# Kernel optimization log

Hardware: AMD Instinct MI355X
Metric: run time of the kernel (lower is better)

## Reference

```python
import jax, jax.numpy as jnp
import numpy as np

HEADS, DIM_HEAD = 4, 32
EAF_LAMBDA, EAF_ZMAX = 1.0, 4.0
MIN_SIGMA, MAX_SIGMA = 1.0, 8.0

def _gen_grid(h, w):
    xs = np.linspace(0.0, 1.0, w, dtype=np.float32)
    ys = np.linspace(0.0, 1.0, h, dtype=np.float32)
    gy, gx = np.meshgrid(ys, xs, indexing='ij')
    return np.stack([gx, gy, np.ones_like(gx)], 0)  # [3,h,w]

def setup_inputs():
    key = jax.random.key(0)
    ks = jax.random.split(key, 12)
    B, N, C, D = 4, 6, 128, 128
    Hb, Wb, fh, fw = 25, 25, 24, 48
    inner = HEADS * DIM_HEAD
    # BEV ego-plane grid (same math as BEVEmbedding with bev 200x200, 100m, 3 decoder blocks)
    g = _gen_grid(Hb, Wb)
    g[0] *= 200.0
    g[1] *= 200.0
    V = np.array([[0., -2., 100.], [-2., 0., 100.], [0., 0., 1.]], dtype=np.float32)
    bev_grid = (np.linalg.inv(V) @ g.reshape(3, -1)).reshape(3, Hb, Wb)
    # image plane pixel grid (buffer), scaled to 480x224 image
    ip = _gen_grid(fh, fw)[None]
    ip[:, 0] *= 480.0
    ip[:, 1] *= 224.0
    # cam->world extrinsics: 6 surround cameras on a ring
    E_inv = np.zeros((B, N, 4, 4), dtype=np.float32)
    for n in range(N):
        yaw = 2.0 * np.pi * n / N
        c, s = np.cos(yaw), np.sin(yaw)
        E_inv[:, n, :3, :3] = np.array([[c, -s, 0.], [s, c, 0.], [0., 0., 1.]], dtype=np.float32)
        E_inv[:, n, :3, 3] = np.array([2. * c, 2. * s, 1.6], dtype=np.float32)
        E_inv[:, n, 3, 3] = 1.0
    Kmat = np.array([[260., 0., 240.], [0., 260., 112.], [0., 0., 1.]], dtype=np.float32)
    I_inv = np.broadcast_to(np.linalg.inv(Kmat), (B, N, 3, 3)).astype(np.float32).copy()
    w = lambda k, shape: 0.02 * jax.random.normal(k, shape, dtype=jnp.float32)
    return dict(
        x=jax.random.normal(ks[0], (B, D, Hb, Wb), dtype=jnp.float32),
        feature=jax.random.normal(ks[1], (B, N, C, fh, fw), dtype=jnp.float32),
        I_inv=jnp.asarray(I_inv), E_inv=jnp.asarray(E_inv),
        bev_grid=jnp.asarray(bev_grid), image_plane=jnp.asarray(ip),
        bn_v_g=jnp.ones(C), bn_v_b=jnp.zeros(C), bn_v_m=jnp.zeros(C), bn_v_var=jnp.ones(C),
        conv_v_w=w(ks[2], (D, C)),
        bn_k_g=jnp.ones(C), bn_k_b=jnp.zeros(C), bn_k_m=jnp.zeros(C), bn_k_var=jnp.ones(C),
        conv_k_w=w(ks[3], (D, C)),
        ln_q_g=jnp.ones(D), ln_q_b=jnp.zeros(D),
        ln_k_g=jnp.ones(D), ln_k_b=jnp.zeros(D),
        ln_v_g=jnp.ones(D), ln_v_b=jnp.zeros(D),
        Wq=w(ks[4], (inner, D)), bq=jnp.zeros(inner),
        Wk=w(ks[5], (inner, D)), bk=jnp.zeros(inner),
        Wv=w(ks[6], (inner, D)), bv=jnp.zeros(inner),
        Wo=w(ks[7], (D, inner)), bo=jnp.zeros(D),
        ln_pre_g=jnp.ones(D), ln_pre_b=jnp.zeros(D),
        W1=w(ks[8], (2 * D, D)), b1=jnp.zeros(2 * D),
        W2=w(ks[9], (D, 2 * D)), b2=jnp.zeros(D),
        ln_post_g=jnp.ones(D), ln_post_b=jnp.zeros(D),
    )

def _ln(x, g, b):
    m = x.mean(-1, keepdims=True)
    v = ((x - m) ** 2).mean(-1, keepdims=True)
    return (x - m) * jax.lax.rsqrt(v + 1e-5) * g + b

def _bn_relu_conv(f, g, b, mu, var, Wc):
    # inference BatchNorm2d -> ReLU -> 1x1 Conv (no bias)
    f = (f - mu[None, :, None, None]) * (jax.lax.rsqrt(var + 1e-5) * g)[None, :, None, None] + b[None, :, None, None]
    f = jax.nn.relu(f)
    return jnp.einsum('bchw,dc->bdhw', f, Wc)

def reference(x, feature, I_inv, E_inv, bev_grid, image_plane,
              bn_v_g, bn_v_b, bn_v_m, bn_v_var, conv_v_w,
              bn_k_g, bn_k_b, bn_k_m, bn_k_var, conv_k_w,
              ln_q_g, ln_q_b, ln_k_g, ln_k_b, ln_v_g, ln_v_b,
              Wq, bq, Wk, bk, Wv, bv, Wo, bo,
              ln_pre_g, ln_pre_b, W1, b1, W2, b2, ln_post_g, ln_post_b):
    B, N, C, fh, fw = feature.shape
    _, D, Hb, Wb = x.shape
    Q = Hb * Wb
    Kp = fh * fw
    feat = feature.reshape(B * N, C, fh, fw)
    val = _bn_relu_conv(feat, bn_v_g, bn_v_b, bn_v_m, bn_v_var, conv_v_w)
    keyf = _bn_relu_conv(feat, bn_k_g, bn_k_b, bn_k_m, bn_k_var, conv_k_w)
    v = val.reshape(B, N, D, fh, fw)
    k = keyf.reshape(B, N, D, fh, fw)
    # ---- EAF weights ----
    xy = bev_grid[:2].reshape(2, Q).T                      # [Q,2]
    ones = jnp.ones((Q, 1), dtype=bev_grid.dtype)
    P0 = jnp.concatenate([xy, 0.0 * ones, ones], -1)       # [Q,4] z=0
    P1 = jnp.concatenate([xy, EAF_ZMAX * ones, ones], -1)  # [Q,4] z=zmax
    E = jnp.linalg.inv(E_inv)                              # world->cam
    P0c = jnp.einsum('bnij,qj->bnqi', E, P0)
    P1c = jnp.einsum('bnij,qj->bnqi', E, P1)
    Icam = jnp.linalg.inv(I_inv)
    p0 = jnp.einsum('bnij,bnqj->bnqi', Icam, P0c[..., :3])
    p1 = jnp.einsum('bnij,bnqj->bnqi', Icam, P1c[..., :3])
    p0 = p0 / (p0[..., 2:3] + 1e-8)
    p1 = p1 / (p1[..., 2:3] + 1e-8)
    l = jnp.cross(p0, p1)                                  # epipolar line [B,N,Q,3]
    denom = jnp.maximum(jnp.sqrt(l[..., 0] ** 2 + l[..., 1] ** 2), 1e-8)
    l_hat = l / denom[..., None]
    x_img = image_plane[0].reshape(3, Kp).T                # [K,3]
    d = jnp.abs(jnp.einsum('bnqj,kj->bnqk', l_hat, x_img))
    # adaptive lambda_{q,i}
    cam_xy = E_inv[..., :2, 3]                             # [B,N,2]
    vec = xy[None, None] - cam_xy[:, :, None]              # [B,N,Q,2]
    dist = jnp.linalg.norm(vec, axis=-1) + 1e-6
    dist_max = dist.max(axis=(1, 2), keepdims=True) + 1e-6
    dist_norm = jnp.clip(dist / dist_max, 0.0, 1.0)
    sigma = MAX_SIGMA - dist_norm * (MAX_SIGMA - MIN_SIGMA)
    lambda_qi = 1.0 / (sigma + 1e-6)
    scale_w = (EAF_LAMBDA * lambda_qi) ** 2                # [B,N,Q]
    Wmask = jnp.exp(-scale_w[..., None] * d ** 2)          # [B,N,Q,K]
    W_logits = Wmask.transpose(0, 2, 1, 3).reshape(B, Q, N * Kp)
    # ---- cross attention (EAF weight multiplied into logits pre-softmax) ----
    qt = x.reshape(B, D, Q).transpose(0, 2, 1)             # [B,Q,D]
    kt = k.transpose(0, 1, 3, 4, 2).reshape(B, N * Kp, D)
    vt = v.transpose(0, 1, 3, 4, 2).reshape(B, N * Kp, D)
    qp = _ln(qt, ln_q_g, ln_q_b) @ Wq.T + bq
    kp = _ln(kt, ln_k_g, ln_k_b) @ Wk.T + bk
    vp = _ln(vt, ln_v_g, ln_v_b) @ Wv.T + bv
    qh = qp.reshape(B, Q, HEADS, DIM_HEAD).transpose(0, 2, 1, 3)
    kh = kp.reshape(B, N * Kp, HEADS, DIM_HEAD).transpose(0, 2, 1, 3)
    vh = vp.reshape(B, N * Kp, HEADS, DIM_HEAD).transpose(0, 2, 1, 3)
    logits = jnp.einsum('bhqd,bhkd->bhqk', qh, kh) * (DIM_HEAD ** -0.5)
    logits = logits * W_logits[:, None]                    # broadcast over heads
    attn = jax.nn.softmax(logits, axis=-1)
    out = jnp.einsum('bhqk,bhkd->bhqd', attn, vh)
    out = out.transpose(0, 2, 1, 3).reshape(B, Q, HEADS * DIM_HEAD)
    out = out @ Wo.T + bo                                  # [B,Q,D]
    z = out + qt                                           # skip = x
    z = _ln(z, ln_pre_g, ln_pre_b)
    z = z + (jax.nn.gelu(z @ W1.T + b1, approximate=False) @ W2.T + b2)
    z = _ln(z, ln_post_g, ln_post_b)
    return z.transpose(0, 2, 1).reshape(B, D, Hb, Wb)
```

## Files before the change

kernel.cpp:

```cpp
#include <hip/hip_runtime.h>
#include <hip/hip_bf16.h>

typedef unsigned short u16;
typedef __attribute__((ext_vector_type(8))) short short8v;
typedef __attribute__((ext_vector_type(4))) float f32x4;
typedef __attribute__((ext_vector_type(2))) __fp16 fp16x2;

#define B_   4
#define N_   6
#define Q_   625
#define QPAD 640
#define KP_  1152
#define NK_  6912
#define NKB  216
#define NSPLIT 24
#define KSEG (NK_/NSPLIT)
#define FHW  1152
#define LOG2E 1.4426950408889634f
#define LOG2_LOG2E 0.5287663729448977f

__device__ __forceinline__ float bfu(unsigned int u16v){ return __uint_as_float(u16v << 16); }
__device__ __forceinline__ unsigned int f2bfu(float f){
  unsigned int u = __float_as_uint(f);
  return (u + 0x7fffu + ((u>>16)&1u)) >> 16;
}
__device__ __forceinline__ float exp2a(float x){
  float r; asm("v_exp_f32 %0, %1" : "=v"(r) : "v"(x)); return r;
}
__device__ __forceinline__ unsigned cvtpk_bf16(float lo, float hi){
  unsigned r; asm("v_cvt_pk_bf16_f32 %0, %1, %2" : "=v"(r) : "v"(lo), "v"(hi)); return r;
}
__device__ __forceinline__ unsigned cvtpk_f16(float lo, float hi){
  union { fp16x2 h; unsigned u; } c;
  c.h = __builtin_amdgcn_cvt_pkrtz(lo, hi);
  return c.u;
}
__device__ __forceinline__ float ldfeat(const void* p, size_t i, bool isbf){
  return isbf ? bfu((unsigned)reinterpret_cast<const u16*>(p)[i])
              : reinterpret_cast<const float*>(p)[i];
}
union U4S8 { uint4 u; short8v s; };
union H2U { unsigned u; fp16x2 h; };

struct InPack {
  const void* p[38];
  int off[38];
  int sz[38];
  int nseg;
  int total;
};

__global__ __launch_bounds__(256) void k_ingest(InPack P, float* __restrict__ dst,
                                                const unsigned* __restrict__ magic,
                                                u16* __restrict__ wbf,
                                                float* __restrict__ csK, float* __restrict__ cbK,
                                                float* __restrict__ csV, float* __restrict__ cbV){
  int idx = blockIdx.x*256 + threadIdx.x;
  bool isbf = (*magic == 0x3F803F80u);
  if (idx < P.total){
    int lo=0, hi=P.nseg-1;
    while (lo<hi){ int mid=(lo+hi+1)>>1; if (P.off[mid]<=idx) lo=mid; else hi=mid-1; }
    int j = idx - P.off[lo];
    float v = 0.f;
    if (j < P.sz[lo]) v = ldfeat(P.p[lo], j, isbf);
    dst[idx] = v;
    return;
  }
  int e = idx - P.total;
  if (e < 81920){
    int mat = e >> 14, i = e & 16383;
    int srcIdx = mat==0?15: mat==1?10: mat==2?24: mat==3?26: 22;
    wbf[e] = (u16)f2bfu(ldfeat(P.p[srcIdx], i, isbf));
  } else if (e < 98304){
    wbf[e] = (u16)f2bfu(ldfeat(P.p[28], e-81920, isbf));
  } else if (e < 131072){
    wbf[e] = (u16)f2bfu(ldfeat(P.p[32], e-98304, isbf));
  } else if (e < 163840){
    wbf[e] = (u16)f2bfu(ldfeat(P.p[34], e-131072, isbf));
  } else if (e < 163840+128){
    int c = e - 163840;
    float g = ldfeat(P.p[11], c, isbf), bb = ldfeat(P.p[12], c, isbf);
    float m = ldfeat(P.p[13], c, isbf), vv = ldfeat(P.p[14], c, isbf);
    float s = rsqrtf(vv+1e-5f)*g;
    csK[c]=s; cbK[c]=bb - m*s;
  } else if (e < 163840+256){
    int c = e - 163840 - 128;
    float g = ldfeat(P.p[6], c, isbf), bb = ldfeat(P.p[7], c, isbf);
    float m = ldfeat(P.p[8], c, isbf), vv = ldfeat(P.p[9], c, isbf);
    float s = rsqrtf(vv+1e-5f)*g;
    csV[c]=s; cbV[c]=bb - m*s;
  }
}

__global__ void k_distmax(const float* __restrict__ bev, const float* __restrict__ Einv,
                          float* __restrict__ dmax)
{
  int b = blockIdx.x, tid = threadIdx.x;
  float mx = 0.f;
  for (int i = tid; i < N_*Q_; i += 256){
    int n = i / Q_, q = i - n*Q_;
    float x = bev[q], y = bev[Q_+q];
    float cx = Einv[(b*N_+n)*16 + 3], cy = Einv[(b*N_+n)*16 + 7];
    float dx = x-cx, dy = y-cy;
    mx = fmaxf(mx, sqrtf(dx*dx+dy*dy) + 1e-6f);
  }
  __shared__ float red[256];
  red[tid]=mx; __syncthreads();
  for (int s=128;s>0;s>>=1){ if (tid<s) red[tid]=fmaxf(red[tid],red[tid+s]); __syncthreads(); }
  if (tid==0) dmax[b] = red[0] + 1e-6f;
}

__global__ void k_geom(const float* __restrict__ Einv, const float* __restrict__ Iinv,
                       const float* __restrict__ bev, const float* __restrict__ dmax,
                       float* __restrict__ geom)
{
  int idx = blockIdx.x*256 + threadIdx.x;
  if (idx >= B_*N_*Q_) return;
  int b = idx / (N_*Q_), r = idx - b*(N_*Q_), n = r / Q_, q = r - n*Q_;

  float a[4][8];
  #pragma unroll
  for (int i=0;i<4;++i){
    #pragma unroll
    for (int j=0;j<4;++j) a[i][j] = Einv[(b*N_+n)*16 + i*4 + j];
    #pragma unroll
    for (int j=0;j<4;++j) a[i][4+j] = (i==j)?1.f:0.f;
  }
  #pragma unroll
  for (int col=0;col<4;++col){
    float inv = 1.f/a[col][col];
    #pragma unroll
    for (int j=0;j<8;++j) a[col][j]*=inv;
    #pragma unroll
    for (int rr=0;rr<4;++rr) if (rr!=col){
      float f=a[rr][col];
      #pragma unroll
      for (int j=0;j<8;++j) a[rr][j] -= f*a[col][j];
    }
  }
  float E[3][4];
  #pragma unroll
  for (int i=0;i<3;++i)
    #pragma unroll
    for (int j=0;j<4;++j) E[i][j]=a[i][4+j];

  float m9[9];
  #pragma unroll
  for (int i=0;i<9;++i) m9[i] = Iinv[(b*N_+n)*9 + i];
  float c00 =  m9[4]*m9[8]-m9[5]*m9[7];
  float c01 = -(m9[3]*m9[8]-m9[5]*m9[6]);
  float c02 =  m9[3]*m9[7]-m9[4]*m9[6];
  float id = 1.f/(m9[0]*c00 + m9[1]*c01 + m9[2]*c02);
  float Ic[3][3];
  Ic[0][0]=c00*id; Ic[0][1]=-(m9[1]*m9[8]-m9[2]*m9[7])*id; Ic[0][2]=(m9[1]*m9[5]-m9[2]*m9[4])*id;
  Ic[1][0]=c01*id; Ic[1][1]= (m9[0]*m9[8]-m9[2]*m9[6])*id; Ic[1][2]=-(m9[0]*m9[5]-m9[2]*m9[3])*id;
  Ic[2][0]=c02*id; Ic[2][1]=-(m9[0]*m9[7]-m9[1]*m9[6])*id; Ic[2][2]=(m9[0]*m9[4]-m9[1]*m9[3])*id;

  float x = bev[q], y = bev[Q_+q];
  float P0c[3], P1c[3];
  #pragma unroll
  for (int i=0;i<3;++i){
    P0c[i] = E[i][0]*x + E[i][1]*y + E[i][3];
    P1c[i] = E[i][0]*x + E[i][1]*y + E[i][2]*4.0f + E[i][3];
  }
  float p0[3], p1[3];
  #pragma unroll
  for (int i=0;i<3;++i){
    p0[i] = Ic[i][0]*P0c[0] + Ic[i][1]*P0c[1] + Ic[i][2]*P0c[2];
    p1[i] = Ic[i][0]*P1c[0] + Ic[i][1]*P1c[1] + Ic[i][2]*P1c[2];
  }
  float z0 = p0[2]+1e-8f, z1 = p1[2]+1e-8f;
  #pragma unroll
  for (int i=0;i<3;++i){ p0[i]/=z0; p1[i]/=z1; }
  float l0 = p0[1]*p1[2]-p0[2]*p1[1];
  float l1 = p0[2]*p1[0]-p0[0]*p1[2];
  float l2 = p0[0]*p1[1]-p0[1]*p1[0];
  float den = fmaxf(sqrtf(l0*l0+l1*l1), 1e-8f);
  float cx = Einv[(b*N_+n)*16+3], cy = Einv[(b*N_+n)*16+7];
  float dx = x-cx, dy = y-cy;
  float dist = sqrtf(dx*dx+dy*dy) + 1e-6f;
  float dn = fminf(fmaxf(dist/dmax[b], 0.f), 1.f);
  float sigma = 8.0f - dn*7.0f;
  float lam = 1.f/(sigma+1e-6f);
  float* g = geom + (size_t)idx*4;
  g[0]=l0/den; g[1]=l1/den; g[2]=l2/den;
  g[3]=-(lam*lam)*LOG2E;
}

__global__ __launch_bounds__(256) void k_kvproj(
  const void* __restrict__ feat, const unsigned* __restrict__ magic,
  const float* __restrict__ csK, const float* __restrict__ cbK,
  const float* __restrict__ csV, const float* __restrict__ cbV,
  const u16* __restrict__ convKbf, const u16* __restrict__ convVbf,
  const u16* __restrict__ WkBf, const u16* __restrict__ WvBf,
  const float* __restrict__ lkg, const float* __restrict__ lkb,
  const float* __restrict__ lvg, const float* __restrict__ lvb,
  const float* __restrict__ bk_, const float* __restrict__ bv_,
  u16* __restrict__ kp, u16* __restrict__ vpB)
{
  __shared__ __align__(16) unsigned char lds_tile[16384];
  __shared__ float2 redLN[4][64];
  uint4* lds16 = reinterpret_cast<uint4*>(lds_tile);

  const int tid = threadIdx.x;
  const int w = tid >> 6, l = tid & 63;
  const int lr = l & 15, lg4 = l >> 4;
  const int ptile = blockIdx.x;
  const int bn = blockIdx.y, b = bn/6, n = bn - b*6;
  const bool isbf = (*magic == 0x3F803F80u);

  const size_t fbase = (size_t)bn*128*FHW + ptile*64 + l;
  float fv[32];
  #pragma unroll
  for (int pass=0; pass<4; ++pass)
    #pragma unroll
    for (int j=0;j<8;++j){
      int c = pass*32 + w*8 + j;
      fv[pass*8+j] = ldfeat(feat, fbase + (size_t)c*FHW, isbf);
    }

  const int psw = l & 7;
  for (int half=0; half<2; ++half){
    const float* cs   = half ? csV : csK;
    const float* cbv_ = half ? cbV : cbK;
    const u16* convB  = half ? convVbf : convKbf;
    const u16* WB     = half ? WvBf : WkBf;
    const float* lng  = half ? lvg : lkg;
    const float* lnb  = half ? lvb : lkb;
    const float* bias = half ? bv_ : bk_;

    #pragma unroll
    for (int pass=0; pass<4; ++pass){
      int c0 = pass*32 + w*8;
      unsigned int u[4];
      #pragma unroll
      for (int i2=0;i2<4;++i2){
        int ca = c0 + i2*2, cb2 = ca+1;
        float aa = fmaxf(fv[pass*8+i2*2  ]*cs[ca]+cbv_[ca], 0.f);
        float ab = fmaxf(fv[pass*8+i2*2+1]*cs[cb2]+cbv_[cb2], 0.f);
        u[i2] = f2bfu(aa) | (f2bfu(ab)<<16);
      }
      int c8 = c0 >> 3;
      lds16[l*16 + (c8 ^ psw)] = make_uint4(u[0],u[1],u[2],u[3]);
    }
    __syncthreads();

    f32x4 acc[2][4];
    #pragma unroll
    for (int i=0;i<2;++i)
      #pragma unroll
      for (int j=0;j<4;++j) acc[i][j] = (f32x4){0.f,0.f,0.f,0.f};

    #pragma unroll
    for (int ks2=0; ks2<4; ++ks2){
      short8v af[2];
      #pragma unroll
      for (int ib=0; ib<2; ++ib)
        af[ib] = *reinterpret_cast<const short8v*>(convB + ((w*32 + ib*16 + lr)<<7) + (ks2<<5) + (lg4<<3));
      #pragma unroll
      for (int pb2=0; pb2<4; ++pb2){
        int p = pb2*16 + lr;
        U4S8 bu; bu.u = lds16[p*16 + ((ks2*4 + lg4) ^ (p&7))];
        acc[0][pb2] = __builtin_amdgcn_mfma_f32_16x16x32_bf16(af[0], bu.s, acc[0][pb2], 0,0,0);
        acc[1][pb2] = __builtin_amdgcn_mfma_f32_16x16x32_bf16(af[1], bu.s, acc[1][pb2], 0,0,0);
      }
    }

    float s1v[4], s2v[4];
    #pragma unroll
    for (int pb2=0;pb2<4;++pb2){
      float s=0.f, s2=0.f;
      #pragma unroll
      for (int ib=0;ib<2;++ib)
        #pragma unroll
        for (int r=0;r<4;++r){ float v = acc[ib][pb2][r]; s+=v; s2+=v*v; }
      s += __shfl_xor(s,16);  s += __shfl_xor(s,32);
      s2 += __shfl_xor(s2,16); s2 += __shfl_xor(s2,32);
      s1v[pb2]=s; s2v[pb2]=s2;
    }
    if (l < 16){
      #pragma unroll
      for (int pb2=0;pb2<4;++pb2) redLN[w][pb2*16+l] = make_float2(s1v[pb2], s2v[pb2]);
    }
    __syncthreads();

    float mean[4], rstd[4];
    #pragma unroll
    for (int pb2=0;pb2<4;++pb2){
      int p = pb2*16 + lr;
      float2 t0 = redLN[0][p], t1 = redLN[1][p], t2 = redLN[2][p], t3 = redLN[3][p];
      float S = t0.x+t1.x+t2.x+t3.x, S2 = t0.y+t1.y+t2.y+t3.y;
      float mm = S*(1.f/128.f);
      float var = fmaxf(S2*(1.f/128.f) - mm*mm, 0.f);
      mean[pb2] = mm; rstd[pb2] = rsqrtf(var + 1e-5f);
    }
    float4 g4[2], b4[2];
    #pragma unroll
    for (int ib=0;ib<2;++ib){
      g4[ib] = *reinterpret_cast<const float4*>(lng + w*32 + ib*16 + lg4*4);
      b4[ib] = *reinterpret_cast<const float4*>(lnb + w*32 + ib*16 + lg4*4);
    }
    #pragma unroll
    for (int ib=0;ib<2;++ib){
      const float* gg = &g4[ib].x; const float* bb2 = &b4[ib].x;
      int d0 = w*32 + ib*16 + lg4*4;
      int d8 = d0 >> 3, doff = (d0 & 7) * 2;
      #pragma unroll
      for (int pb2=0;pb2<4;++pb2){
        int p = pb2*16 + lr;
        float z0 = (acc[ib][pb2][0]-mean[pb2])*rstd[pb2]*gg[0]+bb2[0];
        float z1 = (acc[ib][pb2][1]-mean[pb2])*rstd[pb2]*gg[1]+bb2[1];
        float z2 = (acc[ib][pb2][2]-mean[pb2])*rstd[pb2]*gg[2]+bb2[2];
        float z3 = (acc[ib][pb2][3]-mean[pb2])*rstd[pb2]*gg[3]+bb2[3];
        unsigned int u0 = f2bfu(z0) | (f2bfu(z1)<<16);
        unsigned int u1 = f2bfu(z2) | (f2bfu(z3)<<16);
        *reinterpret_cast<uint2*>(lds_tile + p*256 + ((d8 ^ (p&7))<<4) + doff) = make_uint2(u0,u1);
      }
    }
    __syncthreads();

    f32x4 acc2[2][4];
    #pragma unroll
    for (int i=0;i<2;++i)
      #pragma unroll
      for (int j=0;j<4;++j) acc2[i][j] = (f32x4){0.f,0.f,0.f,0.f};

    #pragma unroll
    for (int ks2=0; ks2<4; ++ks2){
      short8v af[2];
      #pragma unroll
      for (int ib=0; ib<2; ++ib)
        af[ib] = *reinterpret_cast<const short8v*>(WB + ((w*32 + ib*16 + lr)<<7) + (ks2<<5) + (lg4<<3));
      #pragma unroll
      for (int pb2=0; pb2<4; ++pb2){
        int p = pb2*16 + lr;
        U4S8 bu; bu.u = lds16[p*16 + ((ks2*4 + lg4) ^ (p&7))];
        acc2[0][pb2] = __builtin_amdgcn_mfma_f32_16x16x32_bf16(af[0], bu.s, acc2[0][pb2], 0,0,0);
        acc2[1][pb2] = __builtin_amdgcn_mfma_f32_16x16x32_bf16(af[1], bu.s, acc2[1][pb2], 0,0,0);
      }
    }
    float4 bias4[2];
    #pragma unroll
    for (int ib=0;ib<2;++ib)
      bias4[ib] = *reinterpret_cast<const float4*>(bias + w*32 + ib*16 + lg4*4);

    __syncthreads();

    if (half == 0){
      #pragma unroll
      for (int ib=0;ib<2;++ib){
        const float* bb2 = &bias4[ib].x;
        int i0 = w*32 + ib*16 + lg4*4;
        int i8 = i0 >> 3, ioff = (i0 & 7) * 2;
        #pragma unroll
        for (int pb2=0;pb2<4;++pb2){
          int p = pb2*16 + lr;
          unsigned int u0 = f2bfu(acc2[ib][pb2][0]+bb2[0]) | (f2bfu(acc2[ib][pb2][1]+bb2[1])<<16);
          unsigned int u1 = f2bfu(acc2[ib][pb2][2]+bb2[2]) | (f2bfu(acc2[ib][pb2][3]+bb2[3])<<16);
          *reinterpret_cast<uint2*>(lds_tile + p*256 + ((i8 ^ (p&7))<<4) + ioff) = make_uint2(u0,u1);
        }
      }
      __syncthreads();
      size_t krow0 = (size_t)b*NK_ + n*KP_ + ptile*64;
      #pragma unroll
      for (int kk=0;kk<4;++kk){
        int idx = kk*256 + tid;
        int p = idx >> 4, j = idx & 15;
        uint4 vv = lds16[p*16 + (j ^ (p&7))];
        *reinterpret_cast<uint4*>(kp + (krow0 + p)*128 + j*8) = vv;
      }
    } else {
      u16* lds2 = reinterpret_cast<u16*>(lds_tile);
      #pragma unroll
      for (int ib=0;ib<2;++ib){
        const float* bb2 = &bias4[ib].x;
        int i0 = w*32 + ib*16 + lg4*4;
        #pragma unroll
        for (int pb2=0;pb2<4;++pb2){
          int p = pb2*16 + lr;
          int pc = ((p&12)<<1) | (p&3) | ((p&16)>>2) | (p&32);
          #pragma unroll
          for (int r=0;r<4;++r)
            lds2[(i0+r)*64 + pc] = (u16)f2bfu(acc2[ib][pb2][r]+bb2[r]);
        }
      }
      __syncthreads();
      int kb0 = b*NKB + n*(KP_/32) + ptile*2;
      #pragma unroll
      for (int kk=0;kk<4;++kk){
        int idx = kk*256 + tid;
        int p2 = idx >> 9, d = (idx>>2)&127, ch = idx&3;
        uint4 vv = lds16[d*8 + p2*4 + ch];
        *reinterpret_cast<uint4*>(vpB + ((size_t)(kb0+p2)*128 + d)*32 + ch*8) = vv;
      }
    }
    __syncthreads();
  }
}

__global__ __launch_bounds__(256) void k_qprojM(
  const float* __restrict__ x, const float* __restrict__ lg, const float* __restrict__ lb,
  const u16* __restrict__ WqBf, const float* __restrict__ bq_, u16* __restrict__ qp)
{
  const float SCL = 0.17677669529663687f;
  __shared__ __align__(16) unsigned char lds_tile[16384];
  __shared__ float redS[4][64], redS2[4][64];
  uint4* lds16 = reinterpret_cast<uint4*>(lds_tile);

  const int tid = threadIdx.x;
  const int w = tid >> 6, l = tid & 63;
  const int lr = l & 15, lg4 = l >> 4;
  const int q0 = blockIdx.x * 64;
  const int b  = blockIdx.y;

  int qg = q0 + l; if (qg > Q_-1) qg = Q_-1;
  float xv[32];
  float s = 0.f, s2 = 0.f;
  #pragma unroll
  for (int i=0;i<32;++i){
    float v = x[(size_t)(b*128 + w*32 + i)*Q_ + qg];
    xv[i] = v; s += v; s2 += v*v;
  }
  redS[w][l] = s; redS2[w][l] = s2;
  __syncthreads();
  float S  = redS[0][l]+redS[1][l]+redS[2][l]+redS[3][l];
  float S2 = redS2[0][l]+redS2[1][l]+redS2[2][l]+redS2[3][l];
  float mm = S*(1.f/128.f);
  float rs = rsqrtf(fmaxf(S2*(1.f/128.f)-mm*mm, 0.f) + 1e-5f);
  #pragma unroll
  for (int j=0;j<4;++j){
    unsigned u[4];
    #pragma unroll
    for (int c2=0;c2<4;++c2){
      int i = j*8 + c2*2;
      int d = w*32 + i;
      float z0 = (xv[i]  -mm)*rs*lg[d]   + lb[d];
      float z1 = (xv[i+1]-mm)*rs*lg[d+1] + lb[d+1];
      u[c2] = f2bfu(z0) | (f2bfu(z1)<<16);
    }
    int d8 = w*4 + j;
    lds16[l*16 + (d8 ^ (l&7))] = make_uint4(u[0],u[1],u[2],u[3]);
  }
  __syncthreads();

  f32x4 acc2[2][4];
  #pragma unroll
  for (int i=0;i<2;++i)
    #pragma unroll
    for (int j=0;j<4;++j) acc2[i][j] = (f32x4){0.f,0.f,0.f,0.f};

  #pragma unroll
  for (int ks2=0; ks2<4; ++ks2){
    short8v af[2];
    #pragma unroll
    for (int ib=0; ib<2; ++ib)
      af[ib] = *reinterpret_cast<const short8v*>(WqBf + ((w*32 + ib*16 + lr)<<7) + (ks2<<5) + (lg4<<3));
    #pragma unroll
    for (int pb2=0; pb2<4; ++pb2){
      int p = pb2*16 + lr;
      U4S8 bu; bu.u = lds16[p*16 + ((ks2*4 + lg4) ^ (p&7))];
      acc2[0][pb2] = __builtin_amdgcn_mfma_f32_16x16x32_bf16(af[0], bu.s, acc2[0][pb2], 0,0,0);
      acc2[1][pb2] = __builtin_amdgcn_mfma_f32_16x16x32_bf16(af[1], bu.s, acc2[1][pb2], 0,0,0);
    }
  }
  float4 bias4[2];
  #pragma unroll
  for (int ib=0;ib<2;++ib)
    bias4[ib] = *reinterpret_cast<const float4*>(bq_ + w*32 + ib*16 + lg4*4);

  __syncthreads();
  #pragma unroll
  for (int ib=0;ib<2;++ib){
    const float* bb2 = &bias4[ib].x;
    int i0 = w*32 + ib*16 + lg4*4;
    int i8 = i0 >> 3, ioff = (i0 & 7) * 2;
    #pragma unroll
    for (int pb2=0;pb2<4;++pb2){
      int p = pb2*16 + lr;
      unsigned int u0 = f2bfu((acc2[ib][pb2][0]+bb2[0])*SCL) | (f2bfu((acc2[ib][pb2][1]+bb2[1])*SCL)<<16);
      unsigned int u1 = f2bfu((acc2[ib][pb2][2]+bb2[2])*SCL) | (f2bfu((acc2[ib][pb2][3]+bb2[3])*SCL)<<16);
      *reinterpret_cast<uint2*>(lds_tile + p*256 + ((i8 ^ (p&7))<<4) + ioff) = make_uint2(u0,u1);
    }
  }
  __syncthreads();
  #pragma unroll
  for (int kk=0;kk<4;++kk){
    int idx = kk*256 + tid;
    int p = idx >> 4, j = idx & 15;
    uint4 vv = lds16[p*16 + (j ^ (p&7))];
    *reinterpret_cast<uint4*>(qp + (size_t)(b*QPAD + q0 + p)*128 + j*8) = vv;
  }
}

__global__ __launch_bounds__(256) void k_attn(
    const u16* __restrict__ qp, const u16* __restrict__ kp, const u16* __restrict__ vpB,
    const float* __restrict__ geom, const float* __restrict__ ip,
    float* __restrict__ part)
{
  __shared__ uint4 ldsK[2][512];
  __shared__ u16  ldsW[2][32*36];

  const int tid = threadIdx.x;
  const int h = tid >> 6;
  const int lane = tid & 63;
  const int lq = lane & 15;
  const int g  = lane >> 4;
  const int bid = blockIdx.x;
  const int b = bid / (20*NSPLIT);
  const int r = bid - b*(20*NSPLIT);
  const int qt = r / NSPLIT;
  const int ks = r - qt*NSPLIT;
  const int q0 = qt*32;
  const int qa = q0 + lq;
  const int qb = q0 + 16 + lq;

  short8v bq0 = *reinterpret_cast<const short8v*>(qp + ((size_t)(b*QPAD + qa))*128 + h*32 + g*8);
  short8v bq1 = *reinterpret_cast<const short8v*>(qp + ((size_t)(b*QPAD + qb))*128 + h*32 + g*8);

  f32x4 o00={0,0,0,0}, o01={0,0,0,0}, o10={0,0,0,0}, o11={0,0,0,0};
  f32x4 zero4 = {0.f,0.f,0.f,0.f};
  float psum0 = 0.f, psum1 = 0.f;

  const int kbeg = ks*KSEG, kend = kbeg + KSEG;
  const int n0 = kbeg / KP_;
  const int pb0 = kbeg - n0*KP_;

  const int wq = tid >> 3, wc = tid & 7;
  int qwg = q0 + wq; if (qwg > Q_-1) qwg = Q_-1;
  const float* gw_ = geom + ((size_t)((b*N_+n0)*Q_ + qwg))*4;
  const float wl0 = gw_[0], wl1 = gw_[1], wl2 = gw_[2], wgw = gw_[3];

  const int c2 = tid*2;
  const int kr0 = c2 >> 4, kch = c2 & 15;
  auto STAGE = [&](int buf, int k0){
    const uint4* gk = reinterpret_cast<const uint4*>(kp + (size_t)(b*NK_ + k0)*128);
    uint4 k0v = gk[c2], k1v = gk[c2+1];
    ldsK[buf][kr0*16 + (kch     ^ (kr0&7))] = k0v;
    ldsK[buf][kr0*16 + ((kch+1) ^ (kr0&7))] = k1v;
  };
  auto WSTAGE = [&](int buf, int k0){
    int key = pb0 + (k0 - kbeg) + wc*4;
    float4 xx = *reinterpret_cast<const float4*>(ip + key);
    float4 yy = *reinterpret_cast<const float4*>(ip + KP_ + key);
    const float* xp = &xx.x; const float* yp = &yy.x;
    float wv[4];
    #pragma unroll
    for (int i=0;i<4;++i){
      float dln = fmaf(wl0, xp[i], fmaf(wl1, yp[i], wl2));
      wv[i] = exp2a(fmaf(wgw, dln*dln, LOG2_LOG2E));
    }
    uint2 pk;
    pk.x = cvtpk_f16(wv[0], wv[1]);
    pk.y = cvtpk_f16(wv[2], wv[3]);
    *reinterpret_cast<uint2*>(&ldsW[buf][wq*36 + wc*4]) = pk;
  };

  const uint4* vpb4 = reinterpret_cast<const uint4*>(vpB);
  const int dd = h*32 + lq;
  const int iv0 = dd*4 + g, iv1 = (dd+16)*4 + g;
  auto VPAN = [&](int k0){ return vpb4 + ((size_t)(b*NKB + (k0>>5)))*512; };

  STAGE(0, kbeg);
  WSTAGE(0, kbeg);
  U4S8 vc0, vc1;
  { const uint4* vp = VPAN(kbeg); vc0.u = vp[iv0]; vc1.u = vp[iv1]; }

  int cur = 0;
  const int kchunk = h*4 + g;
  for (int k0 = kbeg; k0 < kend; k0 += 32){
    __syncthreads();
    bool more = (k0 + 32) < kend;
    if (more){ STAGE(cur^1, k0+32); WSTAGE(cur^1, k0+32); }
    int kn = more ? (k0 + 32) : k0;
    U4S8 vn0, vn1;
    { const uint4* vp = VPAN(kn); vn0.u = vp[iv0]; vn1.u = vp[iv1]; }

    uint2 wA0 = *reinterpret_cast<const uint2*>(&ldsW[cur][lq*36 + g*4]);
    uint2 wA1 = *reinterpret_cast<const uint2*>(&ldsW[cur][lq*36 + 16 + g*4]);
    uint2 wB0 = *reinterpret_cast<const uint2*>(&ldsW[cur][(16+lq)*36 + g*4]);
    uint2 wB1 = *reinterpret_cast<const uint2*>(&ldsW[cur][(16+lq)*36 + 16 + g*4]);
    float w00[4], w01[4], w10[4], w11[4];
    {
      H2U t0,t1,t2,t3,t4,t5,t6,t7;
      t0.u=wA0.x; t1.u=wA0.y; t2.u=wA1.x; t3.u=wA1.y;
      t4.u=wB0.x; t5.u=wB0.y; t6.u=wB1.x; t7.u=wB1.y;
      w00[0]=(float)t0.h[0]; w00[1]=(float)t0.h[1]; w00[2]=(float)t1.h[0]; w00[3]=(float)t1.h[1];
      w01[0]=(float)t2.h[0]; w01[1]=(float)t2.h[1]; w01[2]=(float)t3.h[0]; w01[3]=(float)t3.h[1];
      w10[0]=(float)t4.h[0]; w10[1]=(float)t4.h[1]; w10[2]=(float)t5.h[0]; w10[3]=(float)t5.h[1];
      w11[0]=(float)t6.h[0]; w11[1]=(float)t6.h[1]; w11[2]=(float)t7.h[0]; w11[3]=(float)t7.h[1];
    }

    __builtin_amdgcn_s_setprio(1);
    U4S8 a0, a1;
    a0.u = ldsK[cur][lq*16      + (kchunk ^ (lq&7))];
    a1.u = ldsK[cur][(16+lq)*16 + (kchunk ^ (lq&7))];
    f32x4 s00 = __builtin_amdgcn_mfma_f32_16x16x32_bf16(a0.s, bq0, zero4, 0,0,0);
    f32x4 s01 = __builtin_amdgcn_mfma_f32_16x16x32_bf16(a1.s, bq0, zero4, 0,0,0);
    f32x4 s10 = __builtin_amdgcn_mfma_f32_16x16x32_bf16(a0.s, bq1, zero4, 0,0,0);
    f32x4 s11 = __builtin_amdgcn_mfma_f32_16x16x32_bf16(a1.s, bq1, zero4, 0,0,0);

    float p00[4], p01[4], p10[4], p11[4];
    #pragma unroll
    for (int r2=0;r2<4;++r2){
      p00[r2] = exp2a(fmaf(s00[r2], w00[r2], -8.f));
      p01[r2] = exp2a(fmaf(s01[r2], w01[r2], -8.f));
      psum0 += p00[r2] + p01[r2];
      p10[r2] = exp2a(fmaf(s10[r2], w10[r2], -8.f));
      p11[r2] = exp2a(fmaf(s11[r2], w11[r2], -8.f));
      psum1 += p10[r2] + p11[r2];
    }
    union { short8v s; unsigned int u[4]; } bp0, bp1;
    bp0.u[0] = cvtpk_bf16(p00[0], p00[1]);
    bp0.u[1] = cvtpk_bf16(p00[2], p00[3]);
    bp0.u[2] = cvtpk_bf16(p01[0], p01[1]);
    bp0.u[3] = cvtpk_bf16(p01[2], p01[3]);
    bp1.u[0] = cvtpk_bf16(p10[0], p10[1]);
    bp1.u[1] = cvtpk_bf16(p10[2], p10[3]);
    bp1.u[2] = cvtpk_bf16(p11[0], p11[1]);
    bp1.u[3] = cvtpk_bf16(p11[2], p11[3]);

    o00 = __builtin_amdgcn_mfma_f32_16x16x32_bf16(vc0.s, bp0.s, o00, 0,0,0);
    o01 = __builtin_amdgcn_mfma_f32_16x16x32_bf16(vc1.s, bp0.s, o01, 0,0,0);
    o10 = __builtin_amdgcn_mfma_f32_16x16x32_bf16(vc0.s, bp1.s, o10, 0,0,0);
    o11 = __builtin_amdgcn_mfma_f32_16x16x32_bf16(vc1.s, bp1.s, o11, 0,0,0);
    __builtin_amdgcn_s_setprio(0);

    vc0 = vn0; vc1 = vn1;
    cur ^= 1;
  }
  psum0 += __shfl_xor(psum0,16);
  psum0 += __shfl_xor(psum0,32);
  psum1 += __shfl_xor(psum1,16);
  psum1 += __shfl_xor(psum1,32);
  int slot0 = ((b*4 + h)*40 + qt*2    )*NSPLIT + ks;
  int slot1 = ((b*4 + h)*40 + qt*2 + 1)*NSPLIT + ks;
  float* pr0 = part + ((size_t)slot0*16 + lq)*34;
  float* pr1 = part + ((size_t)slot1*16 + lq)*34;
  #pragma unroll
  for (int r2=0;r2<4;++r2){
    pr0[g*4+r2] = o00[r2]; pr0[16+g*4+r2] = o01[r2];
    pr1[g*4+r2] = o10[r2]; pr1[16+g*4+r2] = o11[r2];
  }
  if (g==0){ pr0[33] = psum0; pr1[33] = psum1; }
}

__global__ void k_merge(const float* __restrict__ part, float* __restrict__ ao){
  int idx = blockIdx.x*256 + threadIdx.x;
  if (idx >= B_*4*Q_*32) return;
  int d = idx & 31; int t = idx >> 5; int q = t % Q_; int bh = t / Q_;
  int qt = q >> 4; int qq = q & 15;
  const float* base = part + (size_t)((bh*40+qt)*NSPLIT)*544 + qq*34;
  float num = 0.f, den = 0.f;
  #pragma unroll 4
  for (int s=0;s<NSPLIT;++s){
    num += base[s*544 + d];
    den += base[s*544 + 33];
  }
  int b = bh>>2, h = bh&3;
  ao[((size_t)(b*Q_+q))*128 + h*32 + d] = num/den;
}

__global__ __launch_bounds__(256) void k_epiM(
  const float* __restrict__ ao, const float* __restrict__ x,
  const u16* __restrict__ WoBf, const float* __restrict__ bo_,
  const float* __restrict__ lpg, const float* __restrict__ lpb,
  const u16* __restrict__ W1Bf, const float* __restrict__ b1_,
  const u16* __restrict__ W2Bf, const float* __restrict__ b2_,
  const float* __restrict__ lsg, const float* __restrict__ lsb,
  void* __restrict__ out, const unsigned* __restrict__ magic)
{
  const float ISQ2 = 0.7071067811865476f;
  __shared__ __align__(16) unsigned char lds_tile[16384];
  __shared__ __align__(16) unsigned char lds_h1[32768];
  __shared__ float2 redLN[4][64];
  uint4* lds16 = reinterpret_cast<uint4*>(lds_tile);
  uint4* ldsH  = reinterpret_cast<uint4*>(lds_h1);

  const int tid = threadIdx.x;
  const int w = tid >> 6, l = tid & 63;
  const int lr = l & 15, lg4 = l >> 4;
  const int q0 = blockIdx.x * 64;
  const int b  = blockIdx.y;
  const bool isbf = (*magic == 0x3F803F80u);

  {
    int qg = q0 + l; if (qg > Q_-1) qg = Q_-1;
    const float* ar = ao + ((size_t)(b*Q_+qg))*128 + w*32;
    #pragma unroll
    for (int j=0;j<4;++j){
      float4 v0 = *reinterpret_cast<const float4*>(ar + j*8);
      float4 v1 = *reinterpret_cast<const float4*>(ar + j*8 + 4);
      unsigned u[4];
      u[0] = f2bfu(v0.x) | (f2bfu(v0.y)<<16);
      u[1] = f2bfu(v0.z) | (f2bfu(v0.w)<<16);
      u[2] = f2bfu(v1.x) | (f2bfu(v1.y)<<16);
      u[3] = f2bfu(v1.z) | (f2bfu(v1.w)<<16);
      int d8 = w*4 + j;
      lds16[l*16 + (d8 ^ (l&7))] = make_uint4(u[0],u[1],u[2],u[3]);
    }
  }
  __syncthreads();

  f32x4 acc[2][4];
  #pragma unroll
  for (int i=0;i<2;++i)
    #pragma unroll
    for (int j=0;j<4;++j) acc[i][j] = (f32x4){0.f,0.f,0.f,0.f};
  #pragma unroll
  for (int ks2=0; ks2<4; ++ks2){
    short8v af[2];
    #pragma unroll
    for (int ib=0; ib<2; ++ib)
      af[ib] = *reinterpret_cast<const short8v*>(WoBf + ((w*32 + ib*16 + lr)<<7) + (ks2<<5) + (lg4<<3));
    #pragma unroll
    for (int pb2=0; pb2<4; ++pb2){
      int p = pb2*16 + lr;
      U4S8 bu; bu.u = lds16[p*16 + ((ks2*4 + lg4) ^ (p&7))];
      acc[0][pb2] = __builtin_amdgcn_mfma_f32_16x16x32_bf16(af[0], bu.s, acc[0][pb2], 0,0,0);
      acc[1][pb2] = __builtin_amdgcn_mfma_f32_16x16x32_bf16(af[1], bu.s, acc[1][pb2], 0,0,0);
    }
  }
  float4 bo4[2];
  #pragma unroll
  for (int ib=0;ib<2;++ib)
    bo4[ib] = *reinterpret_cast<const float4*>(bo_ + w*32 + ib*16 + lg4*4);
  f32x4 zv[2][4];
  #pragma unroll
  for (int ib=0;ib<2;++ib){
    const float* bb2 = &bo4[ib].x;
    #pragma unroll
    for (int pb2=0;pb2<4;++pb2){
      int qq2 = q0 + pb2*16 + lr; if (qq2 > Q_-1) qq2 = Q_-1;
      #pragma unroll
      for (int r=0;r<4;++r){
        int i = w*32 + ib*16 + lg4*4 + r;
        zv[ib][pb2][r] = acc[ib][pb2][r] + bb2[r] + x[(size_t)(b*128 + i)*Q_ + qq2];
      }
    }
  }
  float s1v[4], s2v[4];
  #pragma unroll
  for (int pb2=0;pb2<4;++pb2){
    float s=0.f, s2=0.f;
    #pragma unroll
    for (int ib=0;ib<2;++ib)
      #pragma unroll
      for (int r=0;r<4;++r){ float v = zv[ib][pb2][r]; s+=v; s2+=v*v; }
    s += __shfl_xor(s,16);  s += __shfl_xor(s,32);
    s2 += __shfl_xor(s2,16); s2 += __shfl_xor(s2,32);
    s1v[pb2]=s; s2v[pb2]=s2;
  }
  if (l < 16){
    #pragma unroll
    for (int pb2=0;pb2<4;++pb2) redLN[w][pb2*16+l] = make_float2(s1v[pb2], s2v[pb2]);
  }
  __syncthreads();
  float mean1[4], rstd1[4];
  #pragma unroll
  for (int pb2=0;pb2<4;++pb2){
    int p = pb2*16 + lr;
    float2 t0 = redLN[0][p], t1 = redLN[1][p], t2 = redLN[2][p], t3 = redLN[3][p];
    float S = t0.x+t1.x+t2.x+t3.x, S2 = t0.y+t1.y+t2.y+t3.y;
    float mm = S*(1.f/128.f);
    float var = fmaxf(S2*(1.f/128.f) - mm*mm, 0.f);
    mean1[pb2] = mm; rstd1[pb2] = rsqrtf(var + 1e-5f);
  }
  float4 lg4v[2], lb4v[2];
  #pragma unroll
  for (int ib=0;ib<2;++ib){
    lg4v[ib] = *reinterpret_cast<const float4*>(lpg + w*32 + ib*16 + lg4*4);
    lb4v[ib] = *reinterpret_cast<const float4*>(lpb + w*32 + ib*16 + lg4*4);
  }
  #pragma unroll
  for (int ib=0;ib<2;++ib){
    const float* gg = &lg4v[ib].x; const float* bb2 = &lb4v[ib].x;
    int d0 = w*32 + ib*16 + lg4*4;
    int d8 = d0 >> 3, doff = (d0 & 7) * 2;
    #pragma unroll
    for (int pb2=0;pb2<4;++pb2){
      int p = pb2*16 + lr;
      #pragma unroll
      for (int r=0;r<4;++r)
        zv[ib][pb2][r] = (zv[ib][pb2][r]-mean1[pb2])*rstd1[pb2]*gg[r]+bb2[r];
      unsigned int u0 = f2bfu(zv[ib][pb2][0]) | (f2bfu(zv[ib][pb2][1])<<16);
      unsigned int u1 = f2bfu(zv[ib][pb2][2]) | (f2bfu(zv[ib][pb2][3])<<16);
      *reinterpret_cast<uint2*>(lds_tile + p*256 + ((d8 ^ (p&7))<<4) + doff) = make_uint2(u0,u1);
    }
  }
  __syncthreads();

  f32x4 acc1[4][4];
  #pragma unroll
  for (int i=0;i<4;++i)
    #pragma unroll
    for (int j=0;j<4;++j) acc1[i][j] = (f32x4){0.f,0.f,0.f,0.f};
  #pragma unroll
  for (int ks2=0; ks2<4; ++ks2){
    short8v af[4];
    #pragma unroll
    for (int fi=0; fi<4; ++fi)
      af[fi] = *reinterpret_cast<const short8v*>(W1Bf + ((w*64 + fi*16 + lr)<<7) + (ks2<<5) + (lg4<<3));
    #pragma unroll
    for (int pb2=0; pb2<4; ++pb2){
      int p = pb2*16 + lr;
      U4S8 bu; bu.u = lds16[p*16 + ((ks2*4 + lg4) ^ (p&7))];
      #pragma unroll
      for (int fi=0; fi<4; ++fi)
        acc1[fi][pb2] = __builtin_amdgcn_mfma_f32_16x16x32_bf16(af[fi], bu.s, acc1[fi][pb2], 0,0,0);
    }
  }
  #pragma unroll
  for (int fi=0; fi<4; ++fi){
    float4 b14 = *reinterpret_cast<const float4*>(b1_ + w*64 + fi*16 + lg4*4);
    const float* bb2 = &b14.x;
    int i10 = w*64 + fi*16 + lg4*4;
    int ch = i10 >> 3, ioff = (i10 & 7) * 2;
    #pragma unroll
    for (int pb2=0;pb2<4;++pb2){
      int p = pb2*16 + lr;
      float gl[4];
      #pragma unroll
      for (int r=0;r<4;++r){
        float hh = acc1[fi][pb2][r] + bb2[r];
        gl[r] = 0.5f*hh*(1.f+erff(hh*ISQ2));
      }
      unsigned int u0 = f2bfu(gl[0]) | (f2bfu(gl[1])<<16);
      unsigned int u1 = f2bfu(gl[2]) | (f2bfu(gl[3])<<16);
      *reinterpret_cast<uint2*>(lds_h1 + p*512 + ((ch ^ (p&7))<<4) + ioff) = make_uint2(u0,u1);
    }
  }
  __syncthreads();

  f32x4 acc2[2][4];
  #pragma unroll
  for (int i=0;i<2;++i)
    #pragma unroll
    for (int j=0;j<4;++j) acc2[i][j] = (f32x4){0.f,0.f,0.f,0.f};
  #pragma unroll
  for (int ks2=0; ks2<8; ++ks2){
    short8v af[2];
    #pragma unroll
    for (int ib=0; ib<2; ++ib)
      af[ib] = *reinterpret_cast<const short8v*>(W2Bf + (w*32 + ib*16 + lr)*256 + ks2*32 + lg4*8);
    #pragma unroll
    for (int pb2=0; pb2<4; ++pb2){
      int p = pb2*16 + lr;
      U4S8 bu; bu.u = ldsH[p*32 + ((ks2*4 + lg4) ^ (p&7))];
      acc2[0][pb2] = __builtin_amdgcn_mfma_f32_16x16x32_bf16(af[0], bu.s, acc2[0][pb2], 0,0,0);
      acc2[1][pb2] = __builtin_amdgcn_mfma_f32_16x16x32_bf16(af[1], bu.s, acc2[1][pb2], 0,0,0);
    }
  }
  float4 b24[2];
  #pragma unroll
  for (int ib=0;ib<2;++ib)
    b24[ib] = *reinterpret_cast<const float4*>(b2_ + w*32 + ib*16 + lg4*4);
  f32x4 z2[2][4];
  #pragma unroll
  for (int ib=0;ib<2;++ib){
    const float* bb2 = &b24[ib].x;
    #pragma unroll
    for (int pb2=0;pb2<4;++pb2)
      #pragma unroll
      for (int r=0;r<4;++r)
        z2[ib][pb2][r] = zv[ib][pb2][r] + acc2[ib][pb2][r] + bb2[r];
  }
  #pragma unroll
  for (int pb2=0;pb2<4;++pb2){
    float s=0.f, s2=0.f;
    #pragma unroll
    for (int ib=0;ib<2;++ib)
      #pragma unroll
      for (int r=0;r<4;++r){ float v = z2[ib][pb2][r]; s+=v; s2+=v*v; }
    s += __shfl_xor(s,16);  s += __shfl_xor(s,32);
    s2 += __shfl_xor(s2,16); s2 += __shfl_xor(s2,32);
    s1v[pb2]=s; s2v[pb2]=s2;
  }
  __syncthreads();
  if (l < 16){
    #pragma unroll
    for (int pb2=0;pb2<4;++pb2) redLN[w][pb2*16+l] = make_float2(s1v[pb2], s2v[pb2]);
  }
  __syncthreads();
  float4 sg4[2], sb4[2];
  #pragma unroll
  for (int ib=0;ib<2;++ib){
    sg4[ib] = *reinterpret_cast<const float4*>(lsg + w*32 + ib*16 + lg4*4);
    sb4[ib] = *reinterpret_cast<const float4*>(lsb + w*32 + ib*16 + lg4*4);
  }
  #pragma unroll
  for (int pb2=0;pb2<4;++pb2){
    int p = pb2*16 + lr;
    int q = q0 + p;
    if (q >= Q_) continue;
    float2 t0 = redLN[0][p], t1 = redLN[1][p], t2 = redLN[2][p], t3 = redLN[3][p];
    float S = t0.x+t1.x+t2.x+t3.x, S2 = t0.y+t1.y+t2.y+t3.y;
    float mm = S*(1.f/128.f);
    float rs = rsqrtf(fmaxf(S2*(1.f/128.f) - mm*mm, 0.f) + 1e-5f);
    #pragma unroll
    for (int ib=0;ib<2;++ib){
      const float* gg = &sg4[ib].x; const float* bb2 = &sb4[ib].x;
      #pragma unroll
      for (int r=0;r<4;++r){
        int i = w*32 + ib*16 + lg4*4 + r;
        float z3 = (z2[ib][pb2][r]-mm)*rs*gg[r] + bb2[r];
        size_t oidx = (size_t)(b*128+i)*Q_ + q;
        if (isbf) reinterpret_cast<u16*>(out)[oidx] = (u16)f2bfu(z3);
        else      reinterpret_cast<float*>(out)[oidx] = z3;
      }
    }
  }
}

extern "C" void kernel_launch(void* const* d_in, const int* in_sizes, int n_in,
                              void* d_out, int out_size, void* d_ws, size_t ws_size,
                              hipStream_t stream){
  InPack P;
  int nseg = n_in < 38 ? n_in : 38;
  int c = 0;
  for (int i=0;i<nseg;++i){
    P.p[i] = d_in[i];
    P.off[i] = c;
    P.sz[i] = (i == 1) ? 0 : in_sizes[i];
    c += (P.sz[i] + 7) & ~7;
  }
  P.nseg = nseg;
  P.total = c;

  float* fw = (float*)d_ws;
  float* fin = fw;
  const float* fx    = fin + P.off[0];
  const float* fIinv = fin + P.off[2];
  const float* fEinv = fin + P.off[3];
  const float* fbev  = fin + P.off[4];
  const float* fip   = fin + P.off[5];
  const float* flkg  = fin + P.off[18];
  const float* flkb  = fin + P.off[19];
  const float* flvg  = fin + P.off[20];
  const float* flvb  = fin + P.off[21];
  const float* flqg  = fin + P.off[16];
  const float* flqb  = fin + P.off[17];
  const float* fbq   = fin + P.off[23];
  const float* fbk   = fin + P.off[25];
  const float* fbv   = fin + P.off[27];
  const float* fbo   = fin + P.off[29];
  const float* flpg  = fin + P.off[30];
  const float* flpb  = fin + P.off[31];
  const float* fb1   = fin + P.off[33];
  const float* fb2   = fin + P.off[35];
  const float* flsg  = fin + P.off[36];
  const float* flsb  = fin + P.off[37];

  size_t off = (size_t)P.total;
  float* geomW = fin + off;  off += 60000;
  float* dmaxW = fin + off;  off += 8;
  float* csK = fin + off;    off += 128;
  float* cbK = fin + off;    off += 128;
  float* csV = fin + off;    off += 128;
  float* cbV = fin + off;    off += 128;
  float* part = fin + off;   off += (size_t)B_*4*40*NSPLIT*544;
  float* ao   = fin + off;   off += 320000;
  u16* bb = (u16*)(fin + off);
  u16* convKbf = bb;
  u16* convVbf = bb + 16384;
  u16* WkBf    = bb + 32768;
  u16* WvBf    = bb + 49152;
  u16* WqBf    = bb + 65536;
  u16* WoBf    = bb + 81920;
  u16* W1Bf    = bb + 98304;
  u16* W2Bf    = bb + 131072;
  u16* kp  = bb + 163840;
  u16* vpB = kp + (size_t)B_*NK_*128;
  u16* qp  = vpB + (size_t)B_*NK_*128;

  const unsigned* magic = (const unsigned*)d_in[6];
  const void* featRaw = d_in[1];

  int ingestTot = P.total + 163840 + 256;
  k_ingest<<<(ingestTot+255)/256,256,0,stream>>>(P, fin, magic, bb, csK,cbK,csV,cbV);
  k_distmax<<<4,256,0,stream>>>(fbev, fEinv, dmaxW);
  k_geom<<<59,256,0,stream>>>(fEinv, fIinv, fbev, dmaxW, geomW);
  k_kvproj<<<dim3(18,24),256,0,stream>>>(featRaw, magic, csK,cbK,csV,cbV, convKbf,convVbf,
                                         WkBf,WvBf, flkg,flkb,flvg,flvb, fbk,fbv, kp, vpB);
  k_qprojM<<<dim3(10,B_),256,0,stream>>>(fx, flqg,flqb, WqBf, fbq, qp);
  k_attn<<<B_*20*NSPLIT,256,0,stream>>>(qp, kp, vpB, geomW, fip, part);
  k_merge<<<1250,256,0,stream>>>(part, ao);
  k_epiM<<<dim3(10,B_),256,0,stream>>>(ao, fx, WoBf,fbo, flpg,flpb, W1Bf,fb1, W2Bf,fb2,
                                       flsg,flsb, d_out, magic);
}
```

Measured before the change: 97.93 us.

## Fuse distmax into geom kernel and store attention partials in fp16

Merges the per-batch distance-max reduction into the geometry kernel, so every block redundantly computes the max for all four batches, and drops one kernel launch. Attention split partials are now written as fp16 numerators with an fp32 denominator in a padded 40-element row, roughly halving partial-buffer traffic between k_attn and k_merge. The cost is redundant reduction work in every geom block and lower precision in the unnormalized partial outputs.

```diff
diff --git a/kernel.cpp b/kernel.cpp
--- a/kernel.cpp
+++ b/kernel.cpp
@@ -18,6 +18,8 @@
 #define FHW  1152
 #define LOG2E 1.4426950408889634f
 #define LOG2_LOG2E 0.5287663729448977f
+#define SLOT_H 640
+#define ROW_H  40
 
 __device__ __forceinline__ float bfu(unsigned int u16v){ return __uint_as_float(u16v << 16); }
 __device__ __forceinline__ unsigned int f2bfu(float f){
@@ -41,6 +43,7 @@
 }
 union U4S8 { uint4 u; short8v s; };
 union H2U { unsigned u; fp16x2 h; };
+union HU1 { u16 u; __fp16 h; };
 
 struct InPack {
   const void* p[38];
@@ -92,31 +95,39 @@
   }
 }
 
-__global__ void k_distmax(const float* __restrict__ bev, const float* __restrict__ Einv,
-                          float* __restrict__ dmax)
+__global__ __launch_bounds__(256) void k_geom(const float* __restrict__ Einv,
+                                              const float* __restrict__ Iinv,
+                                              const float* __restrict__ bev,
+                                              float* __restrict__ geom)
 {
-  int b = blockIdx.x, tid = threadIdx.x;
-  float mx = 0.f;
+  __shared__ float redm[4][256];
+  int tid = threadIdx.x;
+  float mx[4] = {0.f,0.f,0.f,0.f};
   for (int i = tid; i < N_*Q_; i += 256){
     int n = i / Q_, q = i - n*Q_;
     float x = bev[q], y = bev[Q_+q];
-    float cx = Einv[(b*N_+n)*16 + 3], cy = Einv[(b*N_+n)*16 + 7];
-    float dx = x-cx, dy = y-cy;
-    mx = fmaxf(mx, sqrtf(dx*dx+dy*dy) + 1e-6f);
-  }
-  __shared__ float red[256];
-  red[tid]=mx; __syncthreads();
-  for (int s=128;s>0;s>>=1){ if (tid<s) red[tid]=fmaxf(red[tid],red[tid+s]); __syncthreads(); }
-  if (tid==0) dmax[b] = red[0] + 1e-6f;
-}
-
-__global__ void k_geom(const float* __restrict__ Einv, const float* __restrict__ Iinv,
-                       const float* __restrict__ bev, const float* __restrict__ dmax,
-                       float* __restrict__ geom)
-{
-  int idx = blockIdx.x*256 + threadIdx.x;
+    #pragma unroll
+    for (int bb=0;bb<4;++bb){
+      float cx = Einv[(bb*N_+n)*16 + 3], cy = Einv[(bb*N_+n)*16 + 7];
+      float dx = x-cx, dy = y-cy;
+      mx[bb] = fmaxf(mx[bb], sqrtf(dx*dx+dy*dy) + 1e-6f);
+    }
+  }
+  #pragma unroll
+  for (int bb=0;bb<4;++bb) redm[bb][tid] = mx[bb];
+  __syncthreads();
+  for (int s=128;s>0;s>>=1){
+    if (tid<s){
+      #pragma unroll
+      for (int bb=0;bb<4;++bb) redm[bb][tid] = fmaxf(redm[bb][tid], redm[bb][tid+s]);
+    }
+    __syncthreads();
+  }
+
+  int idx = blockIdx.x*256 + tid;
   if (idx >= B_*N_*Q_) return;
   int b = idx / (N_*Q_), r = idx - b*(N_*Q_), n = r / Q_, q = r - n*Q_;
+  float dmaxv = redm[b][0] + 1e-6f;
 
   float a[4][8];
   #pragma unroll
@@ -179,7 +190,7 @@
   float cx = Einv[(b*N_+n)*16+3], cy = Einv[(b*N_+n)*16+7];
   float dx = x-cx, dy = y-cy;
   float dist = sqrtf(dx*dx+dy*dy) + 1e-6f;
-  float dn = fminf(fmaxf(dist/dmax[b], 0.f), 1.f);
+  float dn = fminf(fmaxf(dist/dmaxv, 0.f), 1.f);
   float sigma = 8.0f - dn*7.0f;
   float lam = 1.f/(sigma+1e-6f);
   float* g = geom + (size_t)idx*4;
@@ -495,7 +506,7 @@
 __global__ __launch_bounds__(256) void k_attn(
     const u16* __restrict__ qp, const u16* __restrict__ kp, const u16* __restrict__ vpB,
     const float* __restrict__ geom, const float* __restrict__ ip,
-    float* __restrict__ part)
+    u16* __restrict__ part)
 {
   __shared__ uint4 ldsK[2][512];
   __shared__ u16  ldsW[2][32*36];
@@ -634,27 +645,34 @@
   psum1 += __shfl_xor(psum1,32);
   int slot0 = ((b*4 + h)*40 + qt*2    )*NSPLIT + ks;
   int slot1 = ((b*4 + h)*40 + qt*2 + 1)*NSPLIT + ks;
-  float* pr0 = part + ((size_t)slot0*16 + lq)*34;
-  float* pr1 = part + ((size_t)slot1*16 + lq)*34;
-  #pragma unroll
-  for (int r2=0;r2<4;++r2){
-    pr0[g*4+r2] = o00[r2]; pr0[16+g*4+r2] = o01[r2];
-    pr1[g*4+r2] = o10[r2]; pr1[16+g*4+r2] = o11[r2];
-  }
-  if (g==0){ pr0[33] = psum0; pr1[33] = psum1; }
-}
-
-__global__ void k_merge(const float* __restrict__ part, float* __restrict__ ao){
+  u16* pr0 = part + (size_t)slot0*SLOT_H + lq*ROW_H;
+  u16* pr1 = part + (size_t)slot1*SLOT_H + lq*ROW_H;
+  *reinterpret_cast<unsigned*>(pr0 + g*4)          = cvtpk_f16(o00[0], o00[1]);
+  *reinterpret_cast<unsigned*>(pr0 + g*4 + 2)      = cvtpk_f16(o00[2], o00[3]);
+  *reinterpret_cast<unsigned*>(pr0 + 16 + g*4)     = cvtpk_f16(o01[0], o01[1]);
+  *reinterpret_cast<unsigned*>(pr0 + 16 + g*4 + 2) = cvtpk_f16(o01[2], o01[3]);
+  *reinterpret_cast<unsigned*>(pr1 + g*4)          = cvtpk_f16(o10[0], o10[1]);
+  *reinterpret_cast<unsigned*>(pr1 + g*4 + 2)      = cvtpk_f16(o10[2], o10[3]);
+  *reinterpret_cast<unsigned*>(pr1 + 16 + g*4)     = cvtpk_f16(o11[0], o11[1]);
+  *reinterpret_cast<unsigned*>(pr1 + 16 + g*4 + 2) = cvtpk_f16(o11[2], o11[3]);
+  if (g==0){
+    *reinterpret_cast<float*>(pr0 + 32) = psum0;
+    *reinterpret_cast<float*>(pr1 + 32) = psum1;
+  }
+}
+
+__global__ void k_merge(const u16* __restrict__ part, float* __restrict__ ao){
   int idx = blockIdx.x*256 + threadIdx.x;
   if (idx >= B_*4*Q_*32) return;
   int d = idx & 31; int t = idx >> 5; int q = t % Q_; int bh = t / Q_;
   int qt = q >> 4; int qq = q & 15;
-  const float* base = part + (size_t)((bh*40+qt)*NSPLIT)*544 + qq*34;
+  const u16* base = part + (size_t)((bh*40+qt)*NSPLIT)*SLOT_H + qq*ROW_H;
   float num = 0.f, den = 0.f;
   #pragma unroll 4
   for (int s=0;s<NSPLIT;++s){
-    num += base[s*544 + d];
-    den += base[s*544 + 33];
+    HU1 hv; hv.u = base[s*SLOT_H + d];
+    num += (float)hv.h;
+    den += *reinterpret_cast<const float*>(base + s*SLOT_H + 32);
   }
   int b = bh>>2, h = bh&3;
   ao[((size_t)(b*Q_+q))*128 + h*32 + d] = num/den;
@@ -952,12 +970,11 @@
 
   size_t off = (size_t)P.total;
   float* geomW = fin + off;  off += 60000;
-  float* dmaxW = fin + off;  off += 8;
   float* csK = fin + off;    off += 128;
   float* cbK = fin + off;    off += 128;
   float* csV = fin + off;    off += 128;
   float* cbV = fin + off;    off += 128;
-  float* part = fin + off;   off += (size_t)B_*4*40*NSPLIT*544;
+  u16* partH = (u16*)(fin + off); off += (size_t)B_*4*40*NSPLIT*(SLOT_H/2);
   float* ao   = fin + off;   off += 320000;
   u16* bb = (u16*)(fin + off);
   u16* convKbf = bb;
@@ -977,13 +994,12 @@
 
   int ingestTot = P.total + 163840 + 256;
   k_ingest<<<(ingestTot+255)/256,256,0,stream>>>(P, fin, magic, bb, csK,cbK,csV,cbV);
-  k_distmax<<<4,256,0,stream>>>(fbev, fEinv, dmaxW);
-  k_geom<<<59,256,0,stream>>>(fEinv, fIinv, fbev, dmaxW, geomW);
+  k_geom<<<59,256,0,stream>>>(fEinv, fIinv, fbev, geomW);
   k_kvproj<<<dim3(18,24),256,0,stream>>>(featRaw, magic, csK,cbK,csV,cbV, convKbf,convVbf,
                                          WkBf,WvBf, flkg,flkb,flvg,flvb, fbk,fbv, kp, vpB);
   k_qprojM<<<dim3(10,B_),256,0,stream>>>(fx, flqg,flqb, WqBf, fbq, qp);
-  k_attn<<<B_*20*NSPLIT,256,0,stream>>>(qp, kp, vpB, geomW, fip, part);
-  k_merge<<<1250,256,0,stream>>>(part, ao);
+  k_attn<<<B_*20*NSPLIT,256,0,stream>>>(qp, kp, vpB, geomW, fip, partH);
+  k_merge<<<1250,256,0,stream>>>(partH, ao);
   k_epiM<<<dim3(10,B_),256,0,stream>>>(ao, fx, WoBf,fbo, flpg,flpb, W1Bf,fb1, W2Bf,fb2,
                                        flsg,flsb, d_out, magic);
 }
```

New measurement: 96.09 us. Within noise of the previous version (-1.9%).
